# Optimization experiments

Hardware: AMD Instinct MI355X
Metric: run time of the kernel (lower is better)

## Reference

```python
import jax, jax.numpy as jnp
import numpy as np

N = 100000   # nodes
E = 1600000  # edges
H = 128      # num_features == hidden_size
C = 64       # num_classes
BN_EPS = 1e-5


def setup_inputs() -> dict:
    key = jax.random.key(0)
    ks = jax.random.split(key, 11)
    return {
        "x": jax.random.normal(ks[0], (N, H), jnp.float32),
        "edge_index": jax.random.randint(ks[1], (2, E), 0, N, dtype=jnp.int32),
        "edge_attr": jax.random.normal(ks[2], (E,), jnp.float32),
        "conv_w": jax.random.normal(ks[3], (2, 3, H, H), jnp.float32) / np.sqrt(H).astype(np.float32),
        "conv_b": jax.random.normal(ks[4], (2, 3, H), jnp.float32) * 0.1,
        "bn_g": jax.random.uniform(ks[5], (2, 3, H), jnp.float32, 0.5, 1.5),
        "bn_b": jax.random.normal(ks[6], (2, 3, H), jnp.float32) * 0.1,
        "bn_m": jax.random.normal(ks[7], (2, 3, H), jnp.float32) * 0.1,
        "bn_v": jax.random.uniform(ks[8], (2, 3, H), jnp.float32, 0.5, 1.5),
        "fc_w": jax.random.normal(ks[9], (H, C), jnp.float32) / np.sqrt(H).astype(np.float32),
        "fc_b": jax.random.normal(ks[10], (C,), jnp.float32) * 0.1,
    }


def _gin_conv(h, edge_index, w, b, g, beta, m, v):
    # GIN: out = MLP((1+eps)*x + sum_{j in N(i)} x_j), eps=0 (PyG default)
    src, dst = edge_index[0], edge_index[1]
    agg = jax.ops.segment_sum(h[src], dst, num_segments=N)  # [N,H] scatter-add
    h = h + agg
    for i in range(3):  # Linear -> BatchNorm1d (eval stats) -> ReLU
        h = h @ w[i] + b[i]
        h = (h - m[i]) * jax.lax.rsqrt(v[i] + BN_EPS) * g[i] + beta[i]
        h = jax.nn.relu(h)
    return h


def reference(x, edge_index, edge_attr, conv_w, conv_b, bn_g, bn_b, bn_m, bn_v, fc_w, fc_b):
    # edge_attr is ignored by default PyG GINConv (no edge weighting in GIN)
    h = jax.nn.relu(_gin_conv(x, edge_index, conv_w[0], conv_b[0], bn_g[0], bn_b[0], bn_m[0], bn_v[0]))
    h = jax.nn.relu(_gin_conv(h, edge_index, conv_w[1], conv_b[1], bn_g[1], bn_b[1], bn_m[1], bn_v[1]))
    # dropout is identity in eval mode
    logits = h @ fc_w + fc_b  # [N,C]
    return jax.nn.log_softmax(logits, axis=1)
```

## Files before the change

### kernel.cpp

```cpp
#include <hip/hip_runtime.h>

#define NN 100000
#define NE 1600000
#define HF 128
#define NC 64
#define AP 136
#define NB 391
#define BSH 8
#define BMASK 255
#define BCAP 4608

typedef __bf16 bf16x8 __attribute__((ext_vector_type(8)));
typedef float  f32x4  __attribute__((ext_vector_type(4)));
typedef float  f32x2  __attribute__((ext_vector_type(2)));
typedef unsigned short us8 __attribute__((ext_vector_type(8)));
typedef unsigned int u32x4 __attribute__((ext_vector_type(4)));

__device__ __forceinline__ unsigned short f2b(float x) {
  unsigned int u = __float_as_uint(x);
  u += 0x7FFFu + ((u >> 16) & 1u);
  return (unsigned short)(u >> 16);
}
__device__ __forceinline__ float b2f(unsigned short b) {
  return __uint_as_float(((unsigned int)b) << 16);
}

__device__ __forceinline__ void addrow(f32x2 acc[4], u32x4 w) {
  #pragma unroll
  for (int i = 0; i < 4; i++) {
    f32x2 p;
    p.x = __uint_as_float(w[i] << 16);
    p.y = __uint_as_float(w[i] & 0xFFFF0000u);
    acc[i] += p;
  }
}

__global__ __launch_bounds__(512) void prologue_bin(const float* __restrict__ x,
                                                    unsigned short* __restrict__ xb,
                                                    const float* __restrict__ conv_w,
                                                    const float* __restrict__ conv_b,
                                                    const float* __restrict__ bn_g,
                                                    const float* __restrict__ bn_b,
                                                    const float* __restrict__ bn_m,
                                                    const float* __restrict__ bn_v,
                                                    const float* __restrict__ fc_w,
                                                    unsigned short* __restrict__ wt,
                                                    unsigned short* __restrict__ wtf,
                                                    float* __restrict__ sarr,
                                                    float* __restrict__ tarr,
                                                    int* __restrict__ gcur,
                                                    const int* __restrict__ src,
                                                    const int* __restrict__ dst,
                                                    unsigned int* __restrict__ binned) {
  __shared__ int hist[NB];
  int t = threadIdx.x;
  int idx = blockIdx.x * 512 + t;
  {
    size_t i = (size_t)idx * 8;
    float4 a = *(const float4*)(x + i);
    float4 b = *(const float4*)(x + i + 4);
    us8 v = { f2b(a.x), f2b(a.y), f2b(a.z), f2b(a.w),
              f2b(b.x), f2b(b.y), f2b(b.z), f2b(b.w) };
    *(us8*)(xb + i) = v;
  }
  if (idx < 3 * HF) {
    int k = idx >> 7, jj = idx & 127;
    xb[(size_t)k * (NN + 1) * HF + (size_t)NN * HF + jj] = 0;
  }
  if (idx < 6 * HF * HF) {
    int j  = idx & 7;
    int m  = (idx >> 3) & 15;
    int q  = (idx >> 7) & 3;
    int nt = (idx >> 9) & 7;
    int k0 = (idx >> 12) & 3;
    int ls = idx >> 14;
    int k = k0 * 32 + q * 8 + j;
    int n = nt * 16 + m;
    wt[idx] = f2b(conv_w[(ls * HF + k) * HF + n]);
  }
  if (idx < HF * NC) {
    int j  = idx & 7;
    int m  = (idx >> 3) & 15;
    int q  = (idx >> 7) & 3;
    int nt = (idx >> 9) & 3;
    int k0 = idx >> 11;
    int k = k0 * 32 + q * 8 + j;
    int c = nt * 16 + m;
    wtf[idx] = f2b(fc_w[k * NC + c]);
  }
  if (idx < 6 * HF) {
    float s = bn_g[idx] * rsqrtf(bn_v[idx] + 1e-5f);
    sarr[idx] = s;
    tarr[idx] = (conv_b[idx] - bn_m[idx]) * s + bn_b[idx];
  }
  if (blockIdx.x < NB) {
    if (t < NB) hist[t] = 0;
    __syncthreads();
    int base = blockIdx.x * 4096;
    int sv[8], dv[8];
    #pragma unroll
    for (int j = 0; j < 8; j++) {
      int e = base + j * 512 + t;
      bool ok = e < NE;
      dv[j] = ok ? dst[e] : -1;
      sv[j] = ok ? src[e] : 0;
      if (ok) atomicAdd(&hist[dv[j] >> BSH], 1);
    }
    __syncthreads();
    if (t < NB) {
      int c = hist[t];
      if (c) hist[t] = t * BCAP + atomicAdd(&gcur[t], c);
    }
    __syncthreads();
    #pragma unroll
    for (int j = 0; j < 8; j++) {
      if (dv[j] >= 0) {
        int b = dv[j] >> BSH;
        int p = atomicAdd(&hist[b], 1);
        binned[p] = (unsigned int)sv[j] | ((unsigned int)(dv[j] & BMASK) << 17);
      }
    }
  }
}

__global__ __launch_bounds__(512) void build_csr(const unsigned int* __restrict__ binned,
                                                 const int* __restrict__ gcur,
                                                 int* __restrict__ offs,
                                                 int* __restrict__ deg,
                                                 int* __restrict__ csr) {
  __shared__ int ncnt[256];
  __shared__ int sm[256];
  int t = threadIdx.x;
  int b = blockIdx.x;
  int beg = b * BCAP;
  int cntb = gcur[b];
  if (t < 256) ncnt[t] = 0;
  __syncthreads();
  for (int e = beg + t; e < beg + cntb; e += 512) atomicAdd(&ncnt[binned[e] >> 17], 1);
  __syncthreads();
  int s = 0;
  if (t < 256) { s = ncnt[t]; sm[t] = s; }
  __syncthreads();
  for (int off = 1; off < 256; off <<= 1) {
    int u = (t < 256 && t >= off) ? sm[t - off] : 0;
    __syncthreads();
    if (t < 256) sm[t] += u;
    __syncthreads();
  }
  if (t < 256) {
    int ex = sm[t] - s + beg;
    int node = (b << BSH) + t;
    if (node < NN) { offs[node] = ex; deg[node] = s; }
    ncnt[t] = ex;
  }
  __syncthreads();
  for (int e = beg + t; e < beg + cntb; e += 512) {
    unsigned int u = binned[e];
    int p = atomicAdd(&ncnt[u >> 17], 1);
    csr[p] = (int)(u & 0x1FFFFu);
  }
}

__global__ __launch_bounds__(256) void aggregate(const unsigned short* __restrict__ h,
                                                 const int* __restrict__ offs,
                                                 const int* __restrict__ deg,
                                                 const int* __restrict__ csr,
                                                 unsigned short* __restrict__ out) {
  int wave = threadIdx.x >> 6;
  int lane = threadIdx.x & 63;
  int node = blockIdx.x * 4 + wave;
  int g  = lane >> 4;
  int sl = lane & 15;
  int beg = offs[node];
  int dg  = deg[node];
  int n  = dg + 1;
  int nf = n < 64 ? n : 64;

  int myidx = NN;
  if (lane < nf) myidx = (lane == dg) ? node : csr[beg + lane];

  f32x2 acc[4];
  #pragma unroll
  for (int i = 0; i < 4; i++) acc[i] = (f32x2){0.f, 0.f};

  int K = (nf + 3) >> 2;
  int j = 0;
  for (; j + 3 < K; j += 4) {
    int s0 = __shfl(myidx, (j + 0) * 4 + g);
    int s1 = __shfl(myidx, (j + 1) * 4 + g);
    int s2 = __shfl(myidx, (j + 2) * 4 + g);
    int s3 = __shfl(myidx, (j + 3) * 4 + g);
    u32x4 v0 = *(const u32x4*)(h + (size_t)s0 * HF + sl * 8);
    u32x4 v1 = *(const u32x4*)(h + (size_t)s1 * HF + sl * 8);
    u32x4 v2 = *(const u32x4*)(h + (size_t)s2 * HF + sl * 8);
    u32x4 v3 = *(const u32x4*)(h + (size_t)s3 * HF + sl * 8);
    addrow(acc, v0);
    addrow(acc, v1);
    addrow(acc, v2);
    addrow(acc, v3);
  }
  for (; j + 1 < K; j += 2) {
    int s0 = __shfl(myidx, (j + 0) * 4 + g);
    int s1 = __shfl(myidx, (j + 1) * 4 + g);
    u32x4 v0 = *(const u32x4*)(h + (size_t)s0 * HF + sl * 8);
    u32x4 v1 = *(const u32x4*)(h + (size_t)s1 * HF + sl * 8);
    addrow(acc, v0);
    addrow(acc, v1);
  }
  if (j < K) {
    int s0 = __shfl(myidx, j * 4 + g);
    u32x4 v0 = *(const u32x4*)(h + (size_t)s0 * HF + sl * 8);
    addrow(acc, v0);
  }

  if (dg >= 64) {
    for (int e = beg + 64 + g; e < beg + dg; e += 4) {
      int s = csr[e];
      u32x4 v = *(const u32x4*)(h + (size_t)s * HF + sl * 8);
      addrow(acc, v);
    }
    if (g == 0) {
      u32x4 v = *(const u32x4*)(h + (size_t)node * HF + sl * 8);
      addrow(acc, v);
    }
  }

  #pragma unroll
  for (int i = 0; i < 4; i++) {
    acc[i].x += __shfl_xor(acc[i].x, 16, 64);
    acc[i].y += __shfl_xor(acc[i].y, 16, 64);
    acc[i].x += __shfl_xor(acc[i].x, 32, 64);
    acc[i].y += __shfl_xor(acc[i].y, 32, 64);
  }
  if (g == 0) {
    us8 r;
    #pragma unroll
    for (int i = 0; i < 4; i++) {
      r[2 * i]     = f2b(acc[i].x);
      r[2 * i + 1] = f2b(acc[i].y);
    }
    *(us8*)(out + (size_t)node * HF + sl * 8) = r;
  }
}

__device__ __forceinline__ void mlp3_body(const unsigned short* __restrict__ in,
                                          unsigned short* Ab,
                                          const unsigned short* __restrict__ wt,
                                          const float* __restrict__ sarr,
                                          const float* __restrict__ tarr,
                                          int layer, int row0, int wave, int lane,
                                          bf16x8 af[4]) {
  int m = lane & 15, q = lane >> 4;
  int node = row0 + wave * 16 + m;
  int nclamp = (node < NN) ? node : 0;
  #pragma unroll
  for (int k0 = 0; k0 < 4; k0++)
    af[k0] = *(const bf16x8*)(in + (size_t)nclamp * HF + k0 * 32 + q * 8);

  const unsigned short* wbase = wt + layer * 3 * 16384;
  #pragma unroll
  for (int sub = 0; sub < 3; sub++) {
    const unsigned short* wsub = wbase + sub * 16384;
    f32x4 acc[8];
    #pragma unroll
    for (int nt = 0; nt < 8; nt++) {
      acc[nt] = (f32x4){0.f, 0.f, 0.f, 0.f};
      #pragma unroll
      for (int k0 = 0; k0 < 4; k0++) {
        bf16x8 bf = *(const bf16x8*)(wsub + ((k0 * 8 + nt) * 64 + lane) * 8);
        acc[nt] = __builtin_amdgcn_mfma_f32_16x16x32_bf16(af[k0], bf, acc[nt], 0, 0, 0);
      }
    }
    const float* sp = sarr + (layer * 3 + sub) * HF;
    const float* tp = tarr + (layer * 3 + sub) * HF;
    #pragma unroll
    for (int nt = 0; nt < 8; nt++) {
      int c = nt * 16 + m;
      float sc = sp[c], sh = tp[c];
      #pragma unroll
      for (int i = 0; i < 4; i++) {
        int r = wave * 16 + q * 4 + i;
        float y = fmaxf(acc[nt][i] * sc + sh, 0.f);
        Ab[r * AP + c] = f2b(y);
      }
    }
    #pragma unroll
    for (int k0 = 0; k0 < 4; k0++)
      af[k0] = *(const bf16x8*)&Ab[(wave * 16 + m) * AP + k0 * 32 + q * 8];
  }
}

__global__ __launch_bounds__(256) void mlp3(const unsigned short* __restrict__ in,
                                            unsigned short* __restrict__ out,
                                            const unsigned short* __restrict__ wt,
                                            const float* __restrict__ sarr,
                                            const float* __restrict__ tarr) {
  __shared__ unsigned short Ab[64 * AP];
  int t = threadIdx.x;
  int lane = t & 63, wave = t >> 6;
  int row0 = blockIdx.x * 64;
  bf16x8 af[4];
  mlp3_body(in, Ab, wt, sarr, tarr, 0, row0, wave, lane, af);

  for (int it = 0; it < 4; it++) {
    int idx = it * 64 + lane;
    int r = wave * 16 + (idx >> 4);
    int c = (idx & 15) << 3;
    int gr = row0 + r;
    if (gr < NN) *(us8*)(out + (size_t)gr * HF + c) = *(const us8*)&Ab[r * AP + c];
  }
}

__global__ __launch_bounds__(256) void mlp3fc(const unsigned short* __restrict__ in,
                                              float* __restrict__ out,
                                              const unsigned short* __restrict__ wt,
                                              const float* __restrict__ sarr,
                                              const float* __restrict__ tarr,
                                              const unsigned short* __restrict__ wtf,
                                              const float* __restrict__ fc_b) {
  __shared__ unsigned short Ab[64 * AP];
  int t = threadIdx.x;
  int lane = t & 63, wave = t >> 6;
  int row0 = blockIdx.x * 64;
  int m = lane & 15, q = lane >> 4;
  bf16x8 af[4];
  mlp3_body(in, Ab, wt, sarr, tarr, 1, row0, wave, lane, af);

  f32x4 acc[4];
  #pragma unroll
  for (int nt = 0; nt < 4; nt++) {
    acc[nt] = (f32x4){0.f, 0.f, 0.f, 0.f};
    #pragma unroll
    for (int k0 = 0; k0 < 4; k0++) {
      bf16x8 bf = *(const bf16x8*)(wtf + ((k0 * 4 + nt) * 64 + lane) * 8);
      acc[nt] = __builtin_amdgcn_mfma_f32_16x16x32_bf16(af[k0], bf, acc[nt], 0, 0, 0);
    }
  }
  float v[4][4];
  #pragma unroll
  for (int nt = 0; nt < 4; nt++) {
    float b = fc_b[nt * 16 + m];
    #pragma unroll
    for (int i = 0; i < 4; i++) v[nt][i] = acc[nt][i] + b;
  }
  float mx[4], sum[4];
  #pragma unroll
  for (int i = 0; i < 4; i++) {
    mx[i] = fmaxf(fmaxf(v[0][i], v[1][i]), fmaxf(v[2][i], v[3][i]));
    mx[i] = fmaxf(mx[i], __shfl_xor(mx[i], 1, 64));
    mx[i] = fmaxf(mx[i], __shfl_xor(mx[i], 2, 64));
    mx[i] = fmaxf(mx[i], __shfl_xor(mx[i], 4, 64));
    mx[i] = fmaxf(mx[i], __shfl_xor(mx[i], 8, 64));
    sum[i] = __expf(v[0][i] - mx[i]) + __expf(v[1][i] - mx[i])
           + __expf(v[2][i] - mx[i]) + __expf(v[3][i] - mx[i]);
    sum[i] += __shfl_xor(sum[i], 1, 64);
    sum[i] += __shfl_xor(sum[i], 2, 64);
    sum[i] += __shfl_xor(sum[i], 4, 64);
    sum[i] += __shfl_xor(sum[i], 8, 64);
    sum[i] = __logf(sum[i]) + mx[i];
  }
  #pragma unroll
  for (int i = 0; i < 4; i++) {
    int gr = row0 + wave * 16 + q * 4 + i;
    if (gr < NN) {
      #pragma unroll
      for (int nt = 0; nt < 4; nt++)
        out[(size_t)gr * NC + nt * 16 + m] = v[nt][i] - sum[i];
    }
  }
}

extern "C" void kernel_launch(void* const* d_in, const int* in_sizes, int n_in,
                              void* d_out, int out_size, void* d_ws, size_t ws_size,
                              hipStream_t stream) {
  const float* x      = (const float*)d_in[0];
  const int*   ei     = (const int*)d_in[1];
  const float* conv_w = (const float*)d_in[3];
  const float* conv_b = (const float*)d_in[4];
  const float* bn_g   = (const float*)d_in[5];
  const float* bn_b   = (const float*)d_in[6];
  const float* bn_m   = (const float*)d_in[7];
  const float* bn_v   = (const float*)d_in[8];
  const float* fc_w   = (const float*)d_in[9];
  const float* fc_b   = (const float*)d_in[10];
  float* out = (float*)d_out;

  const int* srcI = ei;
  const int* dstI = ei + NE;

  unsigned short* Xb   = (unsigned short*)d_ws;
  unsigned short* Abuf = Xb + (size_t)(NN + 1) * HF;
  unsigned short* Bbuf = Abuf + (size_t)(NN + 1) * HF;
  int* gcur   = (int*)(Bbuf + (size_t)(NN + 1) * HF);
  int* offs   = gcur + 512;
  int* deg    = offs + 100004;
  unsigned int* binned = (unsigned int*)(deg + 100004);
  int* csr    = (int*)(binned + (size_t)NB * BCAP);
  unsigned short* wt  = (unsigned short*)(csr + (size_t)NB * BCAP);
  unsigned short* wtf = wt + 6 * HF * HF;
  float* sarr = (float*)(wtf + HF * NC);
  float* tarr = sarr + 6 * HF;

  hipMemsetAsync(gcur, 0, sizeof(int) * NB, stream);
  prologue_bin<<<3125, 512, 0, stream>>>(x, Xb, conv_w, conv_b, bn_g, bn_b, bn_m, bn_v,
                                         fc_w, wt, wtf, sarr, tarr, gcur,
                                         srcI, dstI, binned);
  build_csr<<<NB, 512, 0, stream>>>(binned, gcur, offs, deg, csr);

  aggregate<<<NN / 4, 256, 0, stream>>>(Xb, offs, deg, csr, Abuf);
  mlp3<<<(NN + 63) / 64, 256, 0, stream>>>(Abuf, Bbuf, wt, sarr, tarr);
  aggregate<<<NN / 4, 256, 0, stream>>>(Bbuf, offs, deg, csr, Abuf);
  mlp3fc<<<(NN + 63) / 64, 256, 0, stream>>>(Abuf, out, wt, sarr, tarr, wtf, fc_b);
}
```

Measured before the change: 327.7 us.

## Compute degrees in prologue, stage MLP weights in LDS, split aggregate launches

```diff
diff --git a/kernel.cpp b/kernel.cpp
--- a/kernel.cpp
+++ b/kernel.cpp
@@ -20,9 +20,6 @@
   unsigned int u = __float_as_uint(x);
   u += 0x7FFFu + ((u >> 16) & 1u);
   return (unsigned short)(u >> 16);
-}
-__device__ __forceinline__ float b2f(unsigned short b) {
-  return __uint_as_float(((unsigned int)b) << 16);
 }
 
 __device__ __forceinline__ void addrow(f32x2 acc[4], u32x4 w) {
@@ -49,6 +46,7 @@
                                                     float* __restrict__ sarr,
                                                     float* __restrict__ tarr,
                                                     int* __restrict__ gcur,
+                                                    int* __restrict__ deg,
                                                     const int* __restrict__ src,
                                                     const int* __restrict__ dst,
                                                     unsigned int* __restrict__ binned) {
@@ -93,6 +91,7 @@
     sarr[idx] = s;
     tarr[idx] = (conv_b[idx] - bn_m[idx]) * s + bn_b[idx];
   }
+  atomicAdd(&deg[dst[idx]], 1);
   if (blockIdx.x < NB) {
     if (t < NB) hist[t] = 0;
     __syncthreads();
@@ -125,21 +124,20 @@
 
 __global__ __launch_bounds__(512) void build_csr(const unsigned int* __restrict__ binned,
                                                  const int* __restrict__ gcur,
+                                                 const int* __restrict__ deg,
                                                  int* __restrict__ offs,
-                                                 int* __restrict__ deg,
                                                  int* __restrict__ csr) {
   __shared__ int ncnt[256];
   __shared__ int sm[256];
   int t = threadIdx.x;
   int b = blockIdx.x;
   int beg = b * BCAP;
-  int cntb = gcur[b];
-  if (t < 256) ncnt[t] = 0;
-  __syncthreads();
-  for (int e = beg + t; e < beg + cntb; e += 512) atomicAdd(&ncnt[binned[e] >> 17], 1);
-  __syncthreads();
+  int node = (b << BSH) + (t & 255);
   int s = 0;
-  if (t < 256) { s = ncnt[t]; sm[t] = s; }
+  if (t < 256) {
+    s = (node < NN) ? deg[node] : 0;
+    sm[t] = s;
+  }
   __syncthreads();
   for (int off = 1; off < 256; off <<= 1) {
     int u = (t < 256 && t >= off) ? sm[t - off] : 0;
@@ -149,11 +147,11 @@
   }
   if (t < 256) {
     int ex = sm[t] - s + beg;
-    int node = (b << BSH) + t;
-    if (node < NN) { offs[node] = ex; deg[node] = s; }
+    if (node < NN) offs[node] = ex;
     ncnt[t] = ex;
   }
   __syncthreads();
+  int cntb = gcur[b];
   for (int e = beg + t; e < beg + cntb; e += 512) {
     unsigned int u = binned[e];
     int p = atomicAdd(&ncnt[u >> 17], 1);
@@ -165,10 +163,12 @@
                                                  const int* __restrict__ offs,
                                                  const int* __restrict__ deg,
                                                  const int* __restrict__ csr,
-                                                 unsigned short* __restrict__ out) {
+                                                 unsigned short* __restrict__ out,
+                                                 int nodeBase) {
   int wave = threadIdx.x >> 6;
   int lane = threadIdx.x & 63;
-  int node = blockIdx.x * 4 + wave;
+  int node = nodeBase + blockIdx.x * 4 + wave;
+  if (node >= NN) return;
   int g  = lane >> 4;
   int sl = lane & 15;
   int beg = offs[node];
@@ -245,11 +245,12 @@
 
 __device__ __forceinline__ void mlp3_body(const unsigned short* __restrict__ in,
                                           unsigned short* Ab,
+                                          unsigned short* ws,
                                           const unsigned short* __restrict__ wt,
                                           const float* __restrict__ sarr,
                                           const float* __restrict__ tarr,
                                           int layer, int row0, int wave, int lane,
-                                          bf16x8 af[4]) {
+                                          int t, bf16x8 af[4]) {
   int m = lane & 15, q = lane >> 4;
   int node = row0 + wave * 16 + m;
   int nclamp = (node < NN) ? node : 0;
@@ -261,13 +262,20 @@
   #pragma unroll
   for (int sub = 0; sub < 3; sub++) {
     const unsigned short* wsub = wbase + sub * 16384;
+    __syncthreads();
+    #pragma unroll
+    for (int i = 0; i < 8; i++) {
+      int o = (i * 256 + t) * 8;
+      *(us8*)&ws[o] = *(const us8*)(wsub + o);
+    }
+    __syncthreads();
     f32x4 acc[8];
     #pragma unroll
     for (int nt = 0; nt < 8; nt++) {
       acc[nt] = (f32x4){0.f, 0.f, 0.f, 0.f};
       #pragma unroll
       for (int k0 = 0; k0 < 4; k0++) {
-        bf16x8 bf = *(const bf16x8*)(wsub + ((k0 * 8 + nt) * 64 + lane) * 8);
+        bf16x8 bf = *(const bf16x8*)&ws[((k0 * 8 + nt) * 64 + lane) * 8];
         acc[nt] = __builtin_amdgcn_mfma_f32_16x16x32_bf16(af[k0], bf, acc[nt], 0, 0, 0);
       }
     }
@@ -296,11 +304,12 @@
                                             const float* __restrict__ sarr,
                                             const float* __restrict__ tarr) {
   __shared__ unsigned short Ab[64 * AP];
+  __shared__ unsigned short ws[16384];
   int t = threadIdx.x;
   int lane = t & 63, wave = t >> 6;
   int row0 = blockIdx.x * 64;
   bf16x8 af[4];
-  mlp3_body(in, Ab, wt, sarr, tarr, 0, row0, wave, lane, af);
+  mlp3_body(in, Ab, ws, wt, sarr, tarr, 0, row0, wave, lane, t, af);
 
   for (int it = 0; it < 4; it++) {
     int idx = it * 64 + lane;
@@ -319,12 +328,13 @@
                                               const unsigned short* __restrict__ wtf,
                                               const float* __restrict__ fc_b) {
   __shared__ unsigned short Ab[64 * AP];
+  __shared__ unsigned short ws[16384];
   int t = threadIdx.x;
   int lane = t & 63, wave = t >> 6;
   int row0 = blockIdx.x * 64;
   int m = lane & 15, q = lane >> 4;
   bf16x8 af[4];
-  mlp3_body(in, Ab, wt, sarr, tarr, 1, row0, wave, lane, af);
+  mlp3_body(in, Ab, ws, wt, sarr, tarr, 1, row0, wave, lane, t, af);
 
   f32x4 acc[4];
   #pragma unroll
@@ -392,23 +402,25 @@
   unsigned short* Abuf = Xb + (size_t)(NN + 1) * HF;
   unsigned short* Bbuf = Abuf + (size_t)(NN + 1) * HF;
   int* gcur   = (int*)(Bbuf + (size_t)(NN + 1) * HF);
-  int* offs   = gcur + 512;
-  int* deg    = offs + 100004;
-  unsigned int* binned = (unsigned int*)(deg + 100004);
+  int* deg    = gcur + 512;
+  int* offs   = deg + 100004;
+  unsigned int* binned = (unsigned int*)(offs + 100004);
   int* csr    = (int*)(binned + (size_t)NB * BCAP);
   unsigned short* wt  = (unsigned short*)(csr + (size_t)NB * BCAP);
   unsigned short* wtf = wt + 6 * HF * HF;
   float* sarr = (float*)(wtf + HF * NC);
   float* tarr = sarr + 6 * HF;
 
-  hipMemsetAsync(gcur, 0, sizeof(int) * NB, stream);
+  hipMemsetAsync(gcur, 0, sizeof(int) * (512 + 100004), stream);
   prologue_bin<<<3125, 512, 0, stream>>>(x, Xb, conv_w, conv_b, bn_g, bn_b, bn_m, bn_v,
-                                         fc_w, wt, wtf, sarr, tarr, gcur,
+                                         fc_w, wt, wtf, sarr, tarr, gcur, deg,
                                          srcI, dstI, binned);
-  build_csr<<<NB, 512, 0, stream>>>(binned, gcur, offs, deg, csr);
-
-  aggregate<<<NN / 4, 256, 0, stream>>>(Xb, offs, deg, csr, Abuf);
+  build_csr<<<NB, 512, 0, stream>>>(binned, gcur, deg, offs, csr);
+
+  aggregate<<<12500, 256, 0, stream>>>(Xb, offs, deg, csr, Abuf, 0);
+  aggregate<<<12500, 256, 0, stream>>>(Xb, offs, deg, csr, Abuf, 50000);
   mlp3<<<(NN + 63) / 64, 256, 0, stream>>>(Abuf, Bbuf, wt, sarr, tarr);
-  aggregate<<<NN / 4, 256, 0, stream>>>(Bbuf, offs, deg, csr, Abuf);
+  aggregate<<<12500, 256, 0, stream>>>(Bbuf, offs, deg, csr, Abuf, 0);
+  aggregate<<<12500, 256, 0, stream>>>(Bbuf, offs, deg, csr, Abuf, 50000);
   mlp3fc<<<(NN + 63) / 64, 256, 0, stream>>>(Abuf, out, wt, sarr, tarr, wtf, fc_b);
 }
```

After: 368.4 us. 1.12x slower.
